# Optimization experiments

Measured on AMD Instinct MI355X. Metric: run time of the kernel, lower is better.

Reference implementation:

```python
import jax, jax.numpy as jnp
import numpy as np

TARGET_RADIUS = 0.99

def setup_inputs() -> dict:
    key = jax.random.key(0)
    k1, k2, k3 = jax.random.split(key, 3)
    T, B, D = 2048, 16, 1024
    x = jax.random.normal(k1, (T, B, D), dtype=jnp.float32)
    h0 = jnp.zeros((B, D), dtype=jnp.float32)
    # xavier_uniform for W_x: bound = sqrt(6/(D+D))
    bound = float(np.sqrt(6.0 / (D + D)))
    W_x = jax.random.uniform(k2, (D, D), dtype=jnp.float32, minval=-bound, maxval=bound)
    # d init: uniform(0.9, 0.99)
    d = jax.random.uniform(k3, (D,), dtype=jnp.float32, minval=0.9, maxval=0.99)
    b = jnp.zeros((D,), dtype=jnp.float32)
    return {"x": x, "h0": h0, "W_x": W_x, "d": d, "b": b}

def reference(x, h0, W_x, d, b):
    # Spectral constraint on diagonal recurrence
    d_c = jnp.clip(d, -TARGET_RADIUS, TARGET_RADIUS)
    # Batch the per-timestep input GEMM into one big matmul: [T,B,D] @ [D,D]^T
    xw = jnp.einsum('tbd,ed->tbe', x, W_x) + b  # [T, B, D]

    def step(h_prev, xw_t):
        h_new = jnp.tanh(xw_t + d_c * h_prev)      # [B, D]
        out_t = h_new * jax.nn.silu(h_new)          # self-gating
        return h_new, (h_new, out_t)

    _, (hs, output) = jax.lax.scan(step, h0, xw)
    h = jnp.concatenate([h0[None], hs], axis=0)     # [T+1, B, D]
    return output, h
```

## Files before the change

kernel.cpp:

```cpp
#include <hip/hip_runtime.h>

#define TT 2048
#define BB 16
#define DD 1024
#define BD (BB * DD)

typedef _Float16 f16;
typedef _Float16 f16x8 __attribute__((ext_vector_type(8)));
typedef float f32x4 __attribute__((ext_vector_type(4)));
typedef unsigned int u32;

__device__ __forceinline__ void gload_lds16(const void* g, const void* s) {
    const __attribute__((address_space(1))) u32* gp =
        (const __attribute__((address_space(1))) u32*)(unsigned long long)(size_t)g;
    __attribute__((address_space(3))) u32* sp =
        (__attribute__((address_space(3))) u32*)(u32)(size_t)s;
    __builtin_amdgcn_global_load_lds(gp, sp, 16, 0, 0);
}

__global__ __launch_bounds__(256) void cvt_f16(const float* __restrict__ in,
                                               f16* __restrict__ out, int n8) {
    int i = blockIdx.x * 256 + threadIdx.x;
    const int stride = gridDim.x * 256;
    for (; i < n8; i += stride) {
        const float4* p = (const float4*)in + (size_t)i * 2;
        float4 a = p[0], b = p[1];
        f16x8 o;
        o[0] = (f16)a.x; o[1] = (f16)a.y; o[2] = (f16)a.z; o[3] = (f16)a.w;
        o[4] = (f16)b.x; o[5] = (f16)b.y; o[6] = (f16)b.z; o[7] = (f16)b.w;
        *((f16x8*)out + i) = o;
    }
}

__global__ __launch_bounds__(256) void gemm_f16(const f16* __restrict__ A,
                                                const f16* __restrict__ W,
                                                float* __restrict__ C) {
    __shared__ f16 As[128 * 64];
    __shared__ f16 Bs[128 * 64];

    const int tid = threadIdx.x;
    const int bm = blockIdx.y * 128;
    const int bn = blockIdx.x * 128;

    const int sm = tid >> 3;
    const int ss = tid & 7;
    const int kb = ss ^ (sm & 7);

    const f16* Ag = A + (size_t)(bm + sm) * DD + kb * 8;
    const f16* Bg = W + (size_t)(bn + sm) * DD + kb * 8;

    const int wave = tid >> 6;
    const int lane = tid & 63;
    const int wm = (wave & 1) * 64;
    const int wn = (wave >> 1) * 64;
    const int fr = lane & 15;
    const int quad = lane >> 4;

    f32x4 acc[4][4];
#pragma unroll
    for (int i = 0; i < 4; ++i)
#pragma unroll
        for (int j = 0; j < 4; ++j) acc[i][j] = (f32x4){0.f, 0.f, 0.f, 0.f};

    for (int kt = 0; kt < 16; ++kt) {
        const f16* Agk = Ag + kt * 64;
        const f16* Bgk = Bg + kt * 64;
        __syncthreads();
#pragma unroll
        for (int r = 0; r < 4; ++r) {
            gload_lds16(Agk + (size_t)r * 32 * DD, (const char*)As + (r * 256 + tid) * 16);
            gload_lds16(Bgk + (size_t)r * 32 * DD, (const char*)Bs + (r * 256 + tid) * 16);
        }
        __syncthreads();

#pragma unroll
        for (int ks = 0; ks < 2; ++ks) {
            f16x8 af[4], bf[4];
#pragma unroll
            for (int i = 0; i < 4; ++i) {
                const int row = wm + i * 16 + fr;
                const int slot = (ks * 4 + quad) ^ (row & 7);
                af[i] = *(const f16x8*)((const char*)As + row * 128 + slot * 16);
            }
#pragma unroll
            for (int j = 0; j < 4; ++j) {
                const int row = wn + j * 16 + fr;
                const int slot = (ks * 4 + quad) ^ (row & 7);
                bf[j] = *(const f16x8*)((const char*)Bs + row * 128 + slot * 16);
            }
#pragma unroll
            for (int i = 0; i < 4; ++i)
#pragma unroll
                for (int j = 0; j < 4; ++j)
                    acc[i][j] = __builtin_amdgcn_mfma_f32_16x16x32_f16(af[i], bf[j], acc[i][j], 0, 0, 0);
        }
    }

#pragma unroll
    for (int i = 0; i < 4; ++i) {
        const int gm = bm + wm + i * 16 + quad * 4;
#pragma unroll
        for (int j = 0; j < 4; ++j) {
            const int gn = bn + wn + j * 16 + fr;
            float* cp = C + (size_t)gm * DD + gn;
#pragma unroll
            for (int r = 0; r < 4; ++r)
                cp[(size_t)r * DD] = acc[i][j][r];
        }
    }
}

__device__ __forceinline__ void cell(float vb, float dc, float& h, float& o) {
    const float a = fmaf(dc, h, vb);
    const float E = __expf(2.f * a);
    h = fmaf(-2.f, __builtin_amdgcn_rcpf(E + 1.f), 1.f);
    const float s = __builtin_amdgcn_rcpf(1.f + __expf(-h));
    o = h * h * s;
}

__global__ __launch_bounds__(64) void scan_step(const float* __restrict__ xw,
                                                const float* __restrict__ dvec,
                                                const float* __restrict__ bvec,
                                                const float* __restrict__ h0,
                                                float* __restrict__ out,
                                                float* __restrict__ hout,
                                                int Tc, int first) {
    const int l = blockIdx.x * 64 + threadIdx.x;
    const int e = l & (DD - 1);
    const float dc   = fminf(fmaxf(dvec[e], -0.99f), 0.99f);
    const float bias = bvec[e];

    float h;
    if (first) {
        h = h0[l];
        hout[l] = h;
    } else {
        h = hout[l];
    }

    const float* xp = xw + l;
    float va[16], vb[16];
#pragma unroll
    for (int i = 0; i < 16; ++i) va[i] = xp[(size_t)i * BD] + bias;

    for (int t0 = 0; t0 < Tc; t0 += 32) {
#pragma unroll
        for (int i = 0; i < 16; ++i) vb[i] = xp[(size_t)(t0 + 16 + i) * BD] + bias;
#pragma unroll
        for (int i = 0; i < 16; ++i) {
            float o;
            cell(va[i], dc, h, o);
            __builtin_nontemporal_store(o, out + (size_t)(t0 + i) * BD + l);
            __builtin_nontemporal_store(h, hout + (size_t)(t0 + i + 1) * BD + l);
        }
        if (t0 + 32 < Tc) {
#pragma unroll
            for (int i = 0; i < 16; ++i) va[i] = xp[(size_t)(t0 + 32 + i) * BD] + bias;
        }
#pragma unroll
        for (int i = 0; i < 16; ++i) {
            float o;
            cell(vb[i], dc, h, o);
            __builtin_nontemporal_store(o, out + (size_t)(t0 + 16 + i) * BD + l);
            __builtin_nontemporal_store(h, hout + (size_t)(t0 + 16 + i + 1) * BD + l);
        }
    }
}

extern "C" void kernel_launch(void* const* d_in, const int* in_sizes, int n_in,
                              void* d_out, int out_size, void* d_ws, size_t ws_size,
                              hipStream_t stream) {
    const float* x  = (const float*)d_in[0];
    const float* h0 = (const float*)d_in[1];
    const float* Wx = (const float*)d_in[2];
    const float* dv = (const float*)d_in[3];
    const float* bv = (const float*)d_in[4];

    float* out  = (float*)d_out;
    float* hout = out + (size_t)TT * BD;

    f16* Wf = (f16*)d_ws;
    const size_t wbytes = (size_t)DD * DD * sizeof(f16);
    const size_t rem = (ws_size > wbytes) ? ws_size - wbytes : 0;
    long long Tc = (long long)(rem / ((size_t)BD * 6));
    Tc = (Tc / 64) * 64;
    if (Tc > TT) Tc = TT;
    if (Tc < 64) Tc = 64;

    f16*   xf = (f16*)((char*)d_ws + wbytes);
    float* xw = (float*)((char*)d_ws + wbytes + (size_t)Tc * BD * 2);

    cvt_f16<<<512, 256, 0, stream>>>(Wx, Wf, DD * DD / 8);

    for (int t0 = 0; t0 < TT; ) {
        int tc = (int)Tc;
        if (tc > TT - t0) tc = TT - t0;
        const int n8 = tc * BD / 8;
        cvt_f16<<<2048, 256, 0, stream>>>(x + (size_t)t0 * BD, xf, n8);
        dim3 grid(DD / 128, tc * BB / 128);
        gemm_f16<<<grid, 256, 0, stream>>>(xf, Wf, xw);
        scan_step<<<BD / 64, 64, 0, stream>>>(xw, dv, bv, h0,
                                              out  + (size_t)t0 * BD,
                                              hout + (size_t)t0 * BD,
                                              tc, t0 == 0);
        t0 += tc;
    }
}
```

Baseline: 571.5 us.

## Vectorize scan to two channels per thread and remap GEMM tiles per XCD

The scan kernel now handles two adjacent channels per thread with float2 loads and stores, which halves the number of scan wavefronts and doubles each load's width. The factor of 2 in tanh is folded into pre-scaled d and b to save a multiply per step. The GEMM remaps block indices so each XCD gets a contiguous band of rows, aiming for better L2 reuse of A tiles. The risk is that the scan is latency-bound, so halving its thread count (128 blocks of one wave each) may reduce parallelism on the serial recurrence.

```diff
diff --git a/kernel.cpp b/kernel.cpp
--- a/kernel.cpp
+++ b/kernel.cpp
@@ -8,6 +8,7 @@
 typedef _Float16 f16;
 typedef _Float16 f16x8 __attribute__((ext_vector_type(8)));
 typedef float f32x4 __attribute__((ext_vector_type(4)));
+typedef float f32x2 __attribute__((ext_vector_type(2)));
 typedef unsigned int u32;
 
 __device__ __forceinline__ void gload_lds16(const void* g, const void* s) {
@@ -39,8 +40,13 @@
     __shared__ f16 Bs[128 * 64];
 
     const int tid = threadIdx.x;
-    const int bm = blockIdx.y * 128;
-    const int bn = blockIdx.x * 128;
+
+    const int flat = blockIdx.y * gridDim.x + blockIdx.x;
+    const int xcd = flat & 7;
+    const int j = flat >> 3;
+    const int rows_per_xcd = gridDim.y >> 3;
+    const int bm = (xcd * rows_per_xcd + (j >> 3)) * 128;
+    const int bn = (j & 7) * 128;
 
     const int sm = tid >> 3;
     const int ss = tid & 7;
@@ -60,7 +66,7 @@
 #pragma unroll
     for (int i = 0; i < 4; ++i)
 #pragma unroll
-        for (int j = 0; j < 4; ++j) acc[i][j] = (f32x4){0.f, 0.f, 0.f, 0.f};
+        for (int j2 = 0; j2 < 4; ++j2) acc[i][j2] = (f32x4){0.f, 0.f, 0.f, 0.f};
 
     for (int kt = 0; kt < 16; ++kt) {
         const f16* Agk = Ag + kt * 64;
@@ -83,16 +89,16 @@
                 af[i] = *(const f16x8*)((const char*)As + row * 128 + slot * 16);
             }
 #pragma unroll
-            for (int j = 0; j < 4; ++j) {
-                const int row = wn + j * 16 + fr;
+            for (int j2 = 0; j2 < 4; ++j2) {
+                const int row = wn + j2 * 16 + fr;
                 const int slot = (ks * 4 + quad) ^ (row & 7);
-                bf[j] = *(const f16x8*)((const char*)Bs + row * 128 + slot * 16);
+                bf[j2] = *(const f16x8*)((const char*)Bs + row * 128 + slot * 16);
             }
 #pragma unroll
             for (int i = 0; i < 4; ++i)
 #pragma unroll
-                for (int j = 0; j < 4; ++j)
-                    acc[i][j] = __builtin_amdgcn_mfma_f32_16x16x32_f16(af[i], bf[j], acc[i][j], 0, 0, 0);
+                for (int j2 = 0; j2 < 4; ++j2)
+                    acc[i][j2] = __builtin_amdgcn_mfma_f32_16x16x32_f16(af[i], bf[j2], acc[i][j2], 0, 0, 0);
         }
     }
 
@@ -100,22 +106,26 @@
     for (int i = 0; i < 4; ++i) {
         const int gm = bm + wm + i * 16 + quad * 4;
 #pragma unroll
-        for (int j = 0; j < 4; ++j) {
-            const int gn = bn + wn + j * 16 + fr;
+        for (int j2 = 0; j2 < 4; ++j2) {
+            const int gn = bn + wn + j2 * 16 + fr;
             float* cp = C + (size_t)gm * DD + gn;
 #pragma unroll
             for (int r = 0; r < 4; ++r)
-                cp[(size_t)r * DD] = acc[i][j][r];
-        }
-    }
-}
-
-__device__ __forceinline__ void cell(float vb, float dc, float& h, float& o) {
-    const float a = fmaf(dc, h, vb);
-    const float E = __expf(2.f * a);
-    h = fmaf(-2.f, __builtin_amdgcn_rcpf(E + 1.f), 1.f);
-    const float s = __builtin_amdgcn_rcpf(1.f + __expf(-h));
-    o = h * h * s;
+                cp[(size_t)r * DD] = acc[i][j2][r];
+        }
+    }
+}
+
+__device__ __forceinline__ void cell2(f32x2 v, f32x2 d2, f32x2& h, f32x2& o) {
+#pragma unroll
+    for (int c = 0; c < 2; ++c) {
+        const float z = fmaf(d2[c], h[c], v[c]);
+        const float E = __expf(z);
+        const float t = fmaf(-2.f, __builtin_amdgcn_rcpf(E + 1.f), 1.f);
+        h[c] = t;
+        const float s = __builtin_amdgcn_rcpf(1.f + __expf(-t));
+        o[c] = t * t * s;
+    }
 }
 
 __global__ __launch_bounds__(64) void scan_step(const float* __restrict__ xw,
@@ -125,44 +135,60 @@
                                                 float* __restrict__ out,
                                                 float* __restrict__ hout,
                                                 int Tc, int first) {
-    const int l = blockIdx.x * 64 + threadIdx.x;
+    const int p = blockIdx.x * 64 + threadIdx.x;
+    const int l = p * 2;
     const int e = l & (DD - 1);
-    const float dc   = fminf(fmaxf(dvec[e], -0.99f), 0.99f);
-    const float bias = bvec[e];
-
-    float h;
+
+    const f32x2 dv = *(const f32x2*)(dvec + e);
+    const f32x2 bv = *(const f32x2*)(bvec + e);
+    f32x2 d2, b2;
+    d2.x = 2.f * fminf(fmaxf(dv.x, -0.99f), 0.99f);
+    d2.y = 2.f * fminf(fmaxf(dv.y, -0.99f), 0.99f);
+    b2.x = 2.f * bv.x;
+    b2.y = 2.f * bv.y;
+
+    f32x2 h;
     if (first) {
-        h = h0[l];
-        hout[l] = h;
+        h = *(const f32x2*)(h0 + l);
+        *(f32x2*)(hout + l) = h;
     } else {
-        h = hout[l];
+        h = *(const f32x2*)(hout + l);
     }
 
     const float* xp = xw + l;
-    float va[16], vb[16];
-#pragma unroll
-    for (int i = 0; i < 16; ++i) va[i] = xp[(size_t)i * BD] + bias;
+    f32x2 va[16], vb[16];
+#pragma unroll
+    for (int i = 0; i < 16; ++i) {
+        f32x2 x = *(const f32x2*)(xp + (size_t)i * BD);
+        va[i] = x + x + b2;
+    }
 
     for (int t0 = 0; t0 < Tc; t0 += 32) {
 #pragma unroll
-        for (int i = 0; i < 16; ++i) vb[i] = xp[(size_t)(t0 + 16 + i) * BD] + bias;
-#pragma unroll
         for (int i = 0; i < 16; ++i) {
-            float o;
-            cell(va[i], dc, h, o);
-            __builtin_nontemporal_store(o, out + (size_t)(t0 + i) * BD + l);
-            __builtin_nontemporal_store(h, hout + (size_t)(t0 + i + 1) * BD + l);
+            f32x2 x = *(const f32x2*)(xp + (size_t)(t0 + 16 + i) * BD);
+            vb[i] = x + x + b2;
+        }
+#pragma unroll
+        for (int i = 0; i < 16; ++i) {
+            f32x2 o;
+            cell2(va[i], d2, h, o);
+            __builtin_nontemporal_store(o, (f32x2*)(out + (size_t)(t0 + i) * BD + l));
+            __builtin_nontemporal_store(h, (f32x2*)(hout + (size_t)(t0 + i + 1) * BD + l));
         }
         if (t0 + 32 < Tc) {
 #pragma unroll
-            for (int i = 0; i < 16; ++i) va[i] = xp[(size_t)(t0 + 32 + i) * BD] + bias;
+            for (int i = 0; i < 16; ++i) {
+                f32x2 x = *(const f32x2*)(xp + (size_t)(t0 + 32 + i) * BD);
+                va[i] = x + x + b2;
+            }
         }
 #pragma unroll
         for (int i = 0; i < 16; ++i) {
-            float o;
-            cell(vb[i], dc, h, o);
-            __builtin_nontemporal_store(o, out + (size_t)(t0 + 16 + i) * BD + l);
-            __builtin_nontemporal_store(h, hout + (size_t)(t0 + 16 + i + 1) * BD + l);
+            f32x2 o;
+            cell2(vb[i], d2, h, o);
+            __builtin_nontemporal_store(o, (f32x2*)(out + (size_t)(t0 + 16 + i) * BD + l));
+            __builtin_nontemporal_store(h, (f32x2*)(hout + (size_t)(t0 + 16 + i + 1) * BD + l));
         }
     }
 }
@@ -199,10 +225,10 @@
         cvt_f16<<<2048, 256, 0, stream>>>(x + (size_t)t0 * BD, xf, n8);
         dim3 grid(DD / 128, tc * BB / 128);
         gemm_f16<<<grid, 256, 0, stream>>>(xf, Wf, xw);
-        scan_step<<<BD / 64, 64, 0, stream>>>(xw, dv, bv, h0,
-                                              out  + (size_t)t0 * BD,
-                                              hout + (size_t)t0 * BD,
-                                              tc, t0 == 0);
+        scan_step<<<BD / 128, 64, 0, stream>>>(xw, dv, bv, h0,
+                                               out  + (size_t)t0 * BD,
+                                               hout + (size_t)t0 * BD,
+                                               tc, t0 == 0);
         t0 += tc;
     }
 }
```

New measurement: 601.6 us. +5.3%, slower.
